# Optimization experiments

Measured on AMD Instinct MI355X. Metric: run time of the kernel, lower is better.

The kernel has to match this reference:

```python
import math
import jax, jax.numpy as jnp
import numpy as np

B, A, M, NC = 32, 8400, 32, 80
TOP_K, ALPHA, BETA, EPS = 13, 1.0, 6.0, 1e-9
IMG = 640.0


def _ciou(b1, b2, eps=1e-7):
    # b1, b2 broadcastable [..., 4]; CIoU as in compute_iou (box1=gt, box2=pred)
    b1x1, b1y1, b1x2, b1y2 = b1[..., 0], b1[..., 1], b1[..., 2], b1[..., 3]
    b2x1, b2y1, b2x2, b2y2 = b2[..., 0], b2[..., 1], b2[..., 2], b2[..., 3]
    w1, h1 = b1x2 - b1x1, b1y2 - b1y1 + eps
    w2, h2 = b2x2 - b2x1, b2y2 - b2y1 + eps
    inter = (jnp.minimum(b1x2, b2x2) - jnp.maximum(b1x1, b2x1)).clip(0) * \
            (jnp.minimum(b1y2, b2y2) - jnp.maximum(b1y1, b2y1)).clip(0)
    union = w1 * h1 + w2 * h2 - inter + eps
    iou = inter / union
    cw = jnp.maximum(b1x2, b2x2) - jnp.minimum(b1x1, b2x1)
    ch = jnp.maximum(b1y2, b2y2) - jnp.minimum(b1y1, b2y1)
    c2 = cw ** 2 + ch ** 2 + eps
    rho2 = ((b2x1 + b2x2 - b1x1 - b1x2) ** 2 + (b2y1 + b2y2 - b1y1 - b1y2) ** 2) / 4.0
    v = (4.0 / math.pi ** 2) * (jnp.arctan(w2 / h2) - jnp.arctan(w1 / h1)) ** 2
    alpha = jax.lax.stop_gradient(v / (v - iou + (1.0 + eps)))
    return iou - (rho2 / c2 + v * alpha)


def setup_inputs() -> dict:
    key = jax.random.key(0)
    ks = jax.random.split(key, 8)
    pd_scores = jax.random.uniform(ks[0], (B, A, NC), jnp.float32)
    anc_points = jax.random.uniform(ks[1], (A, 2), jnp.float32) * IMG
    # predicted boxes around anchor points (valid x1<x2, y1<y2)
    off = jax.random.uniform(ks[2], (B, A, 4), jnp.float32) * 80.0 + 2.0
    pd_bboxes = jnp.concatenate([anc_points[None] - off[..., :2],
                                 anc_points[None] + off[..., 2:]], -1)
    # GT boxes: random centers and sizes, clipped to image
    c = jax.random.uniform(ks[3], (B, M, 2), jnp.float32) * IMG
    wh = jax.random.uniform(ks[4], (B, M, 2), jnp.float32) * 180.0 + 20.0
    gt_bboxes = jnp.concatenate([(c - wh / 2).clip(0, IMG), (c + wh / 2).clip(0, IMG)], -1)
    gt_labels = jax.random.randint(ks[5], (B, M, 1), 0, NC, jnp.int64)
    n_valid = jax.random.randint(ks[6], (B,), 1, M + 1)
    mask_gt = (jnp.arange(M)[None, :] < n_valid[:, None]).astype(jnp.float32)[..., None]
    return {"pd_scores": pd_scores, "pd_bboxes": pd_bboxes, "anc_points": anc_points,
            "gt_labels": gt_labels, "gt_bboxes": gt_bboxes, "mask_gt": mask_gt}


def reference(pd_scores, pd_bboxes, anc_points, gt_labels, gt_bboxes, mask_gt):
    b, a, nc = pd_scores.shape
    m = gt_bboxes.shape[1]
    dtype = pd_scores.dtype

    # anchors-inside-GT mask: [B,M,A]
    lt = gt_bboxes[:, :, None, :2]          # [B,M,1,2]
    rb = gt_bboxes[:, :, None, 2:]
    deltas = jnp.concatenate([anc_points[None, None] - lt,
                              rb - anc_points[None, None]], -1)  # [B,M,A,4]
    mask_in_gts = deltas.min(-1) > EPS
    mg = mask_gt[..., 0] > 0                 # [B,M] bool
    gt_mask = mask_in_gts & mg[:, :, None]

    # per-GT class score gather: pd_scores[b, :, gt_labels[b,m]] -> [B,M,A]
    labels = gt_labels[..., 0]               # [B,M]
    idx = jnp.broadcast_to(labels[:, :, None, None], (b, m, a, 1))
    gathered = jnp.take_along_axis(jnp.broadcast_to(pd_scores[:, None], (b, m, a, nc)), idx, axis=3)[..., 0]
    bbox_scores = jnp.where(gt_mask, gathered, 0.0)

    # CIoU overlaps (dense, masked) [B,M,A]
    iou = _ciou(gt_bboxes[:, :, None, :], pd_bboxes[:, None, :, :])
    overlaps = jnp.where(gt_mask, jnp.maximum(iou, 0.0), 0.0)

    align_metric = bbox_scores ** ALPHA * overlaps ** BETA

    # top-k selection with duplicate suppression (faithful to scatter_add loop)
    _, tk_idx = jax.lax.top_k(align_metric, TOP_K)      # [B,M,K]
    tk_mask = jnp.broadcast_to(mg[:, :, None], tk_idx.shape)
    tk_idx = jnp.where(tk_mask, tk_idx, 0)
    bi = jnp.arange(b)[:, None, None]
    mi = jnp.arange(m)[None, :, None]
    counts = jnp.zeros((b, m, a), jnp.int32).at[bi, mi, tk_idx].add(1)
    mask_top_k = jnp.where(counts > 1, 0, counts).astype(dtype)

    mask_pos = mask_top_k * mask_in_gts.astype(dtype) * mg[:, :, None].astype(dtype)
    fg_mask = mask_pos.sum(1)                            # [B,A]

    # resolve anchors assigned to multiple GTs (no-op when none; matches torch branch)
    mask_multi = fg_mask[:, None, :] > 1                 # [B,M,A] (broadcast)
    max_idx = overlaps.argmax(1)                         # [B,A]
    is_max = (jnp.arange(m)[None, :, None] == max_idx[:, None, :]).astype(dtype)
    mask_pos = jnp.where(mask_multi, is_max, mask_pos)
    fg_mask = mask_pos.sum(1)

    target_gt_idx = mask_pos.argmax(1)                   # [B,A]
    target_labels = jnp.maximum(jnp.take_along_axis(labels, target_gt_idx, axis=1), 0)
    target_bboxes = jnp.take_along_axis(
        gt_bboxes, jnp.broadcast_to(target_gt_idx[..., None], (b, a, 4)), axis=1)

    target_scores = jax.nn.one_hot(target_labels, NC, dtype=dtype)
    target_scores = jnp.where((fg_mask > 0)[..., None], target_scores, 0.0)

    am = align_metric * mask_pos
    pos_am = am.max(-1, keepdims=True)                   # [B,M,1]
    pos_ov = (overlaps * mask_pos).max(-1, keepdims=True)
    norm = (am * pos_ov / (pos_am + EPS)).max(1)[..., None]  # [B,A,1]
    target_scores = target_scores * norm

    return target_bboxes, target_scores, fg_mask > 0
```

## Files before the change

### kernel.cpp

```cpp
#include <hip/hip_runtime.h>
#include <math.h>

#define BB 32
#define AA 8400
#define MM 32
#define NCC 80
#define TOPK 13
#define CAP 1024
#define NW (AA / 32 + 1)
#define K12T 512

typedef float nfloat4 __attribute__((ext_vector_type(4)));

__device__ __forceinline__ void wave_argmax(float& v, int& i) {
    #pragma unroll
    for (int off = 32; off > 0; off >>= 1) {
        float ov = __shfl_xor(v, off, 64);
        int oi = __shfl_xor(i, off, 64);
        if (ov > v || (ov == v && oi < i)) { v = ov; i = oi; }
    }
}

__global__ __launch_bounds__(256) void k0_zero(unsigned int* __restrict__ selmask) {
    int g = blockIdx.x * 256 + threadIdx.x;
    if (g < BB * AA / 4) reinterpret_cast<uint4*>(selmask)[g] = uint4{0u, 0u, 0u, 0u};
}

__global__ __launch_bounds__(K12T) void k12_topk(
        const float* __restrict__ pd_scores, const float* __restrict__ pd_bboxes,
        const float* __restrict__ anc, const int* __restrict__ gt_labels,
        const float* __restrict__ gt_bboxes, const float* __restrict__ mask_gt,
        unsigned int* __restrict__ selmask, float* __restrict__ pos_am, float* __restrict__ pos_ov) {
    __shared__ float lval[CAP];
    __shared__ int   lidx[CAP];
    __shared__ unsigned int bmask[NW];
    __shared__ float wv[8];
    __shared__ int   wi[8];
    __shared__ int   wsum[8];
    __shared__ int   s_p;
    const float eps = 1e-7f;
    int ib = blockIdx.x;
    int b = (ib & 7) + ((ib >> 8) << 3);
    int m = (ib >> 3) & 31;
    int bm = b * MM + m;
    unsigned int mbit = 1u << m;
    int tid = threadIdx.x;
    int lane = tid & 63;
    int wid = tid >> 6;
    if (tid == 0) pos_am[bm] = 0.f;
    if (tid == 1) pos_ov[bm] = 0.f;
    if (tid == 2) s_p = 0;
    if (!(mask_gt[bm] > 0.f)) return;

    for (int i = tid; i < NW; i += K12T) bmask[i] = 0u;
    float4 g = reinterpret_cast<const float4*>(gt_bboxes)[bm];

    const float4* anc4 = reinterpret_cast<const float4*>(anc);
    float4 av[9];
    #pragma unroll
    for (int j = 0; j < 9; j++) {
        int e = tid + (j << 9);
        av[j] = anc4[e > 4199 ? 4199 : e];
    }
    unsigned int bits = 0u;
    int c_t = 0;
    #pragma unroll
    for (int j = 0; j < 9; j++) {
        int e = tid + (j << 9);
        bool valid = e < 4200;
        float d0 = fminf(fminf(av[j].x - g.x, av[j].y - g.y), fminf(g.z - av[j].x, g.w - av[j].y));
        float d1 = fminf(fminf(av[j].z - g.x, av[j].w - g.y), fminf(g.z - av[j].z, g.w - av[j].w));
        if (valid && d0 > 1e-9f) { bits |= 1u << (2 * j);     c_t++; }
        if (valid && d1 > 1e-9f) { bits |= 1u << (2 * j + 1); c_t++; }
    }
    int x = c_t;
    #pragma unroll
    for (int off = 1; off < 64; off <<= 1) {
        int y = __shfl_up(x, off, 64);
        if (lane >= off) x += y;
    }
    if (lane == 63) wsum[wid] = x;
    __syncthreads();
    int base = 0, tot = 0;
    #pragma unroll
    for (int w = 0; w < 8; w++) { if (w < wid) base += wsum[w]; tot += wsum[w]; }
    int n_c = min(tot, CAP);
    {
        int o = base + x - c_t;
        unsigned int mm_ = bits;
        while (mm_) {
            int k = __builtin_ctz(mm_);
            mm_ &= mm_ - 1u;
            int i = 2 * tid + ((k >> 1) << 10) + (k & 1);
            if (o < CAP) lidx[o] = i;
            o++;
        }
    }
    for (int s = n_c + tid; s < CAP; s += K12T) { lval[s] = -1.f; lidx[s] = AA; }
    __syncthreads();

    float w1 = g.z - g.x, h1 = g.w - g.y + eps;
    float atg = atanf(w1 / h1);
    float w1h1 = w1 * h1;
    float sgx = g.x + g.z, sgy = g.y + g.w;
    int lab = gt_labels[bm];
    const float4* pbb = reinterpret_cast<const float4*>(pd_bboxes) + (long)b * AA;
    const float* scp = pd_scores + (long)b * AA * NCC + lab;
    int nit = (n_c + K12T - 1) >> 9;
    for (int it = 0; it < nit; it++) {
        int s = (it << 9) + tid;
        bool pos = false;
        if (s < n_c) {
            int i = lidx[s];
            float4 pb = pbb[i];
            float sc = scp[(long)i * NCC];
            float w2 = pb.z - pb.x, h2 = pb.w - pb.y + eps;
            float iw = fmaxf(fminf(g.z, pb.z) - fmaxf(g.x, pb.x), 0.f);
            float ih = fmaxf(fminf(g.w, pb.w) - fmaxf(g.y, pb.y), 0.f);
            float inter = iw * ih;
            float uni = w1h1 + w2 * h2 - inter + eps;
            float iou = inter / uni;
            float cw = fmaxf(g.z, pb.z) - fminf(g.x, pb.x);
            float ch = fmaxf(g.w, pb.w) - fminf(g.y, pb.y);
            float c2 = cw * cw + ch * ch + eps;
            float dx = pb.x + pb.z - sgx, dy = pb.y + pb.w - sgy;
            float rho2 = (dx * dx + dy * dy) * 0.25f;
            float dv = atanf(w2 / h2) - atg;
            float v = 0.4052847345693511f * dv * dv;
            float alpha = v / (v - iou + (1.0f + eps));
            float cv = iou - (rho2 / c2 + v * alpha);
            float ov = fmaxf(cv, 0.f);
            float o2 = ov * ov;
            float val = sc * o2 * o2 * o2;
            pos = val > 0.f;
            lval[s] = pos ? val : -1.f;
            if (pos) atomicOr(&bmask[i >> 5], 1u << (i & 31));
        }
        unsigned long long pm = __ballot(pos);
        if (lane == 0) atomicAdd(&s_p, (int)__popcll(pm));
    }
    __syncthreads();
    int p = s_p;

    if (p >= TOPK) {
        float v0 = lval[tid], v1 = lval[tid + 512];
        int   i0 = lidx[tid], i1 = lidx[tid + 512];
        int mysel = -1;
        for (int k = 0; k < TOPK; k++) {
            float bv = v0; int bi = i0;
            if (v1 > bv || (v1 == bv && i1 < bi)) { bv = v1; bi = i1; }
            wave_argmax(bv, bi);
            if (lane == 0) { wv[wid] = bv; wi[wid] = bi; }
            __syncthreads();
            float gv = wv[0]; int gi = wi[0];
            #pragma unroll
            for (int w = 1; w < 8; w++) {
                float ov = wv[w]; int oi = wi[w];
                if (ov > gv || (ov == gv && oi < gi)) { gv = ov; gi = oi; }
            }
            if (tid == k) mysel = gi;
            if (i0 == gi) v0 = -1.f;
            if (i1 == gi) v1 = -1.f;
            __syncthreads();
        }
        if (tid < TOPK) atomicOr(&selmask[b * AA + mysel], mbit);
    } else {
        for (int s = tid; s < n_c; s += K12T)
            if (lval[s] > 0.f) atomicOr(&selmask[b * AA + lidx[s]], mbit);
        if (wid == 0) {
            int need = TOPK - p;
            for (int base_i = 0; need > 0 && base_i < AA; base_i += 64) {
                int i = base_i + lane;
                bool cand = (i < AA) && !((bmask[i >> 5] >> (i & 31)) & 1u);
                unsigned long long wm = __ballot(cand);
                int take = min(need, (int)__popcll(wm));
                if (cand && (int)__popcll(wm & ((1ull << lane) - 1ull)) < take) {
                    float2 an = reinterpret_cast<const float2*>(anc)[i];
                    float dmin = fminf(fminf(an.x - g.x, an.y - g.y), fminf(g.z - an.x, g.w - an.y));
                    if (dmin > 1e-9f) atomicOr(&selmask[b * AA + i], mbit);
                }
                need -= take;
            }
        }
    }
}

__global__ __launch_bounds__(256) void k3_resolve(
        const float* __restrict__ pd_scores, const float* __restrict__ pd_bboxes,
        const float* __restrict__ anc, const int* __restrict__ gt_labels,
        const float* __restrict__ gt_bboxes, const float* __restrict__ mask_gt,
        const unsigned int* __restrict__ selmask,
        float* __restrict__ pos_am, float* __restrict__ pos_ov,
        float* __restrict__ out_bbox, float* __restrict__ out_fg,
        int2* __restrict__ meta) {
    __shared__ float sg[MM][8];
    __shared__ int slab[MM];
    __shared__ int smg[MM];
    const float eps = 1e-7f;
    int b = blockIdx.y;
    int tid = threadIdx.x;
    if (tid < MM) {
        int gm = b * MM + tid;
        float4 g = reinterpret_cast<const float4*>(gt_bboxes)[gm];
        float w1 = g.z - g.x, h1 = g.w - g.y + eps;
        sg[tid][0] = g.x; sg[tid][1] = g.y; sg[tid][2] = g.z; sg[tid][3] = g.w;
        sg[tid][4] = w1 * h1;
        sg[tid][5] = atanf(w1 / h1);
        sg[tid][6] = g.x + g.z;
        sg[tid][7] = g.y + g.w;
        int lb = gt_labels[gm]; if (lb < 0) lb = 0;
        slab[tid] = lb;
        smg[tid] = mask_gt[gm] > 0.f ? 1 : 0;
    }
    __syncthreads();
    int a = blockIdx.x * 256 + tid;
    if (a >= AA) return;
    int g = b * AA + a;
    unsigned int sel = selmask[g];
    int fg = __popc(sel);

    int tg = 0; bool fgo = false; float ovt = 0.f;
    if (fg >= 1) {
        float ax = anc[a * 2], ay = anc[a * 2 + 1];
        float4 pb = reinterpret_cast<const float4*>(pd_bboxes)[g];
        float w2 = pb.z - pb.x, h2 = pb.w - pb.y + eps;
        float atp = atanf(w2 / h2);
        float w2h2 = w2 * h2;
        float spx = pb.x + pb.z, spy = pb.y + pb.w;
        fgo = true;
        if (fg == 1) {
            tg = __ffs(sel) - 1;
            float gx1 = sg[tg][0], gy1 = sg[tg][1], gx2 = sg[tg][2], gy2 = sg[tg][3];
            float iw = fmaxf(fminf(gx2, pb.z) - fmaxf(gx1, pb.x), 0.f);
            float ih = fmaxf(fminf(gy2, pb.w) - fmaxf(gy1, pb.y), 0.f);
            float inter = iw * ih;
            float uni = sg[tg][4] + w2h2 - inter + eps;
            float iou = inter / uni;
            float cw = fmaxf(gx2, pb.z) - fminf(gx1, pb.x);
            float ch = fmaxf(gy2, pb.w) - fminf(gy1, pb.y);
            float c2 = cw * cw + ch * ch + eps;
            float dx = spx - sg[tg][6], dy = spy - sg[tg][7];
            float rho2 = (dx * dx + dy * dy) * 0.25f;
            float dv = atp - sg[tg][5];
            float v = 0.4052847345693511f * dv * dv;
            float alpha = v / (v - iou + (1.0f + eps));
            ovt = fmaxf(iou - (rho2 / c2 + v * alpha), 0.f);
        } else {
            float bestov = -1.f; int bestm = 0;
            for (int mm = 0; mm < MM; mm++) {
                float gx1 = sg[mm][0], gy1 = sg[mm][1], gx2 = sg[mm][2], gy2 = sg[mm][3];
                float dmin = fminf(fminf(ax - gx1, ay - gy1), fminf(gx2 - ax, gy2 - ay));
                float ov = 0.f;
                if ((dmin > 1e-9f) && smg[mm]) {
                    float iw = fmaxf(fminf(gx2, pb.z) - fmaxf(gx1, pb.x), 0.f);
                    float ih = fmaxf(fminf(gy2, pb.w) - fmaxf(gy1, pb.y), 0.f);
                    float inter = iw * ih;
                    float uni = sg[mm][4] + w2h2 - inter + eps;
                    float iou = inter / uni;
                    float cw = fmaxf(gx2, pb.z) - fminf(gx1, pb.x);
                    float ch = fmaxf(gy2, pb.w) - fminf(gy1, pb.y);
                    float c2 = cw * cw + ch * ch + eps;
                    float dx = spx - sg[mm][6], dy = spy - sg[mm][7];
                    float rho2 = (dx * dx + dy * dy) * 0.25f;
                    float dv = atp - sg[mm][5];
                    float v = 0.4052847345693511f * dv * dv;
                    float alpha = v / (v - iou + (1.0f + eps));
                    ov = fmaxf(iou - (rho2 / c2 + v * alpha), 0.f);
                }
                if (ov > bestov) { bestov = ov; bestm = mm; }
            }
            tg = bestm; ovt = bestov;
        }
    }

    nfloat4 gb = {sg[tg][0], sg[tg][1], sg[tg][2], sg[tg][3]};
    __builtin_nontemporal_store(gb, reinterpret_cast<nfloat4*>(out_bbox) + g);
    out_fg[g] = fgo ? 1.f : 0.f;
    float amv = 0.f;
    if (fgo) {
        float sc = pd_scores[(long)g * NCC + slab[tg]];
        float o2 = ovt * ovt;
        amv = sc * o2 * o2 * o2;
        atomicMax((int*)&pos_am[b * MM + tg], __float_as_int(amv));
        atomicMax((int*)&pos_ov[b * MM + tg], __float_as_int(ovt));
    }
    meta[g] = make_int2(__float_as_int(amv), tg | (slab[tg] << 8) | ((fgo ? 1 : 0) << 16));
}

__global__ __launch_bounds__(256) void k4_scores(
        const int2* __restrict__ meta,
        const float* __restrict__ pos_am, const float* __restrict__ pos_ov,
        float* __restrict__ out_scores) {
    int g = blockIdx.x * 256 + threadIdx.x;
    const int NQ = NCC / 4;
    if (g >= BB * AA * NQ) return;
    int ba = g / NQ;
    int c0 = (g % NQ) * 4;
    nfloat4 o = {0.f, 0.f, 0.f, 0.f};
    int2 mt = meta[ba];
    int p = mt.y;
    if (p & (1 << 16)) {
        int tg = p & 31, lab = (p >> 8) & 127;
        int b = ba / AA;
        int bm = b * MM + tg;
        float nv = (__int_as_float(mt.x) * pos_ov[bm]) / (pos_am[bm] + 1e-9f);
        int d = lab - c0;
        if (d == 0) o.x = nv; else if (d == 1) o.y = nv;
        else if (d == 2) o.z = nv; else if (d == 3) o.w = nv;
    }
    __builtin_nontemporal_store(o, reinterpret_cast<nfloat4*>(out_scores) + g);
}

extern "C" void kernel_launch(void* const* d_in, const int* in_sizes, int n_in,
                              void* d_out, int out_size, void* d_ws, size_t ws_size,
                              hipStream_t stream) {
    const float* pd_scores = (const float*)d_in[0];
    const float* pd_bboxes = (const float*)d_in[1];
    const float* anc       = (const float*)d_in[2];
    const int*   gt_labels = (const int*)d_in[3];
    const float* gt_bboxes = (const float*)d_in[4];
    const float* mask_gt   = (const float*)d_in[5];

    const long nBA = (long)BB * AA;

    char* ws = (char*)d_ws;
    unsigned int* selmask = (unsigned int*)ws;  ws += nBA * 4;
    float* pos_am = (float*)ws;                 ws += BB * MM * 4;
    float* pos_ov = (float*)ws;                 ws += BB * MM * 4;
    int2*  meta   = (int2*)ws;                  ws += nBA * 8;

    float* out_bbox   = (float*)d_out;
    float* out_scores = out_bbox + nBA * 4;
    float* out_fg     = out_scores + nBA * NCC;

    k0_zero<<<(int)((nBA / 4 + 255) / 256), 256, 0, stream>>>(selmask);
    k12_topk<<<BB * MM, K12T, 0, stream>>>(pd_scores, pd_bboxes, anc, gt_labels,
                                           gt_bboxes, mask_gt, selmask, pos_am, pos_ov);
    dim3 g3((AA + 255) / 256, BB);
    k3_resolve<<<g3, 256, 0, stream>>>(pd_scores, pd_bboxes, anc, gt_labels,
                                       gt_bboxes, mask_gt, selmask, pos_am, pos_ov,
                                       out_bbox, out_fg, meta);
    long nS4 = nBA * (NCC / 4);
    k4_scores<<<(int)((nS4 + 255) / 256), 256, 0, stream>>>(meta, pos_am, pos_ov, out_scores);
}
```

Before: 195.0 us.

## Process two GTs per block and do wave-local top-k selection

The top-k kernel now handles two ground-truth boxes per block. It scans every anchor once, sharing the anchor and predicted-box loads and the predicted-box arctangent between both GTs. The prefix-sum compaction is replaced by shared-memory atomic slot allocation. Top-k selection now runs inside one wave per GT, with 16 values per lane and no block-wide barriers. The cost is that every block loads all predicted boxes rather than only those for candidate anchors, plus contention on the shared-memory atomics.

```diff
diff --git a/kernel.cpp b/kernel.cpp
--- a/kernel.cpp
+++ b/kernel.cpp
@@ -7,8 +7,7 @@
 #define NCC 80
 #define TOPK 13
 #define CAP 1024
-#define NW (AA / 32 + 1)
-#define K12T 512
+#define NW2 ((AA + 31) / 32)
 
 typedef float nfloat4 __attribute__((ext_vector_type(4)));
 
@@ -26,160 +25,141 @@
     if (g < BB * AA / 4) reinterpret_cast<uint4*>(selmask)[g] = uint4{0u, 0u, 0u, 0u};
 }
 
-__global__ __launch_bounds__(K12T) void k12_topk(
+__global__ __launch_bounds__(512) void k12_topk(
         const float* __restrict__ pd_scores, const float* __restrict__ pd_bboxes,
         const float* __restrict__ anc, const int* __restrict__ gt_labels,
         const float* __restrict__ gt_bboxes, const float* __restrict__ mask_gt,
         unsigned int* __restrict__ selmask, float* __restrict__ pos_am, float* __restrict__ pos_ov) {
-    __shared__ float lval[CAP];
-    __shared__ int   lidx[CAP];
-    __shared__ unsigned int bmask[NW];
-    __shared__ float wv[8];
-    __shared__ int   wi[8];
-    __shared__ int   wsum[8];
-    __shared__ int   s_p;
+    __shared__ float lv[2][CAP];
+    __shared__ int   li[2][CAP];
+    __shared__ unsigned int bmask[2][NW2];
+    __shared__ float sg[2][8];
+    __shared__ int   smg[2], slab[2];
+    __shared__ int   cnt[2], pcnt[2];
     const float eps = 1e-7f;
-    int ib = blockIdx.x;
-    int b = (ib & 7) + ((ib >> 8) << 3);
-    int m = (ib >> 3) & 31;
-    int bm = b * MM + m;
-    unsigned int mbit = 1u << m;
+    int blk = blockIdx.x;
+    int b  = blk >> 4;
+    int m0 = (blk & 15) << 1;
     int tid = threadIdx.x;
     int lane = tid & 63;
     int wid = tid >> 6;
-    if (tid == 0) pos_am[bm] = 0.f;
-    if (tid == 1) pos_ov[bm] = 0.f;
-    if (tid == 2) s_p = 0;
-    if (!(mask_gt[bm] > 0.f)) return;
-
-    for (int i = tid; i < NW; i += K12T) bmask[i] = 0u;
-    float4 g = reinterpret_cast<const float4*>(gt_bboxes)[bm];
-
-    const float4* anc4 = reinterpret_cast<const float4*>(anc);
-    float4 av[9];
-    #pragma unroll
-    for (int j = 0; j < 9; j++) {
-        int e = tid + (j << 9);
-        av[j] = anc4[e > 4199 ? 4199 : e];
-    }
-    unsigned int bits = 0u;
-    int c_t = 0;
-    #pragma unroll
-    for (int j = 0; j < 9; j++) {
-        int e = tid + (j << 9);
-        bool valid = e < 4200;
-        float d0 = fminf(fminf(av[j].x - g.x, av[j].y - g.y), fminf(g.z - av[j].x, g.w - av[j].y));
-        float d1 = fminf(fminf(av[j].z - g.x, av[j].w - g.y), fminf(g.z - av[j].z, g.w - av[j].w));
-        if (valid && d0 > 1e-9f) { bits |= 1u << (2 * j);     c_t++; }
-        if (valid && d1 > 1e-9f) { bits |= 1u << (2 * j + 1); c_t++; }
-    }
-    int x = c_t;
-    #pragma unroll
-    for (int off = 1; off < 64; off <<= 1) {
-        int y = __shfl_up(x, off, 64);
-        if (lane >= off) x += y;
-    }
-    if (lane == 63) wsum[wid] = x;
+
+    if (tid < 2) {
+        int bm = b * MM + m0 + tid;
+        pos_am[bm] = 0.f;
+        pos_ov[bm] = 0.f;
+        cnt[tid] = 0; pcnt[tid] = 0;
+        int mgv = mask_gt[bm] > 0.f ? 1 : 0;
+        smg[tid] = mgv;
+        float4 g = reinterpret_cast<const float4*>(gt_bboxes)[bm];
+        float w1 = g.z - g.x, h1 = g.w - g.y + eps;
+        sg[tid][0] = g.x; sg[tid][1] = g.y; sg[tid][2] = g.z; sg[tid][3] = g.w;
+        sg[tid][4] = w1 * h1;
+        sg[tid][5] = atanf(w1 / h1);
+        sg[tid][6] = g.x + g.z;
+        sg[tid][7] = g.y + g.w;
+        slab[tid] = gt_labels[bm];
+    }
+    for (int i = tid; i < 2 * NW2; i += 512) bmask[i >> 8 >> 1][i % NW2] = 0u;
     __syncthreads();
-    int base = 0, tot = 0;
-    #pragma unroll
-    for (int w = 0; w < 8; w++) { if (w < wid) base += wsum[w]; tot += wsum[w]; }
-    int n_c = min(tot, CAP);
-    {
-        int o = base + x - c_t;
-        unsigned int mm_ = bits;
-        while (mm_) {
-            int k = __builtin_ctz(mm_);
-            mm_ &= mm_ - 1u;
-            int i = 2 * tid + ((k >> 1) << 10) + (k & 1);
-            if (o < CAP) lidx[o] = i;
-            o++;
+    for (int i = tid; i < NW2; i += 512) { bmask[0][i] = 0u; bmask[1][i] = 0u; }
+    int mg0 = smg[0], mg1 = smg[1];
+    __syncthreads();
+    if (!mg0 && !mg1) return;
+
+    const float2* anc2 = reinterpret_cast<const float2*>(anc);
+    const float4* pbb = reinterpret_cast<const float4*>(pd_bboxes) + (long)b * AA;
+    const float* scb = pd_scores + (long)b * AA * NCC;
+    #pragma unroll 1
+    for (int j = 0; j < 17; j++) {
+        int i = tid + (j << 9);
+        if (i >= AA) break;
+        float2 an = anc2[i];
+        float4 pb = pbb[i];
+        float w2 = pb.z - pb.x, h2 = pb.w - pb.y + eps;
+        float w2h2 = w2 * h2;
+        float spx = pb.x + pb.z, spy = pb.y + pb.w;
+        float atp = 0.f; bool atp_done = false;
+        #pragma unroll
+        for (int mm = 0; mm < 2; mm++) {
+            if (!(mm ? mg1 : mg0)) continue;
+            float gx1 = sg[mm][0], gy1 = sg[mm][1], gx2 = sg[mm][2], gy2 = sg[mm][3];
+            float dmin = fminf(fminf(an.x - gx1, an.y - gy1), fminf(gx2 - an.x, gy2 - an.y));
+            if (dmin > 1e-9f) {
+                if (!atp_done) { atp = atanf(w2 / h2); atp_done = true; }
+                float iw = fmaxf(fminf(gx2, pb.z) - fmaxf(gx1, pb.x), 0.f);
+                float ih = fmaxf(fminf(gy2, pb.w) - fmaxf(gy1, pb.y), 0.f);
+                float inter = iw * ih;
+                float uni = sg[mm][4] + w2h2 - inter + eps;
+                float iou = inter / uni;
+                float cw = fmaxf(gx2, pb.z) - fminf(gx1, pb.x);
+                float ch = fmaxf(gy2, pb.w) - fminf(gy1, pb.y);
+                float c2 = cw * cw + ch * ch + eps;
+                float dx = spx - sg[mm][6], dy = spy - sg[mm][7];
+                float rho2 = (dx * dx + dy * dy) * 0.25f;
+                float dv = atp - sg[mm][5];
+                float v = 0.4052847345693511f * dv * dv;
+                float alpha = v / (v - iou + (1.0f + eps));
+                float cv = iou - (rho2 / c2 + v * alpha);
+                float ov = fmaxf(cv, 0.f);
+                float sc = scb[(long)i * NCC + slab[mm]];
+                float o2 = ov * ov;
+                float val = sc * o2 * o2 * o2;
+                int slot = atomicAdd(&cnt[mm], 1);
+                bool pos = val > 0.f;
+                if (slot < CAP) { lv[mm][slot] = pos ? val : -1.f; li[mm][slot] = i; }
+                if (pos) {
+                    atomicOr(&bmask[mm][i >> 5], 1u << (i & 31));
+                    atomicAdd(&pcnt[mm], 1);
+                }
+            }
         }
     }
-    for (int s = n_c + tid; s < CAP; s += K12T) { lval[s] = -1.f; lidx[s] = AA; }
     __syncthreads();
 
-    float w1 = g.z - g.x, h1 = g.w - g.y + eps;
-    float atg = atanf(w1 / h1);
-    float w1h1 = w1 * h1;
-    float sgx = g.x + g.z, sgy = g.y + g.w;
-    int lab = gt_labels[bm];
-    const float4* pbb = reinterpret_cast<const float4*>(pd_bboxes) + (long)b * AA;
-    const float* scp = pd_scores + (long)b * AA * NCC + lab;
-    int nit = (n_c + K12T - 1) >> 9;
-    for (int it = 0; it < nit; it++) {
-        int s = (it << 9) + tid;
-        bool pos = false;
-        if (s < n_c) {
-            int i = lidx[s];
-            float4 pb = pbb[i];
-            float sc = scp[(long)i * NCC];
-            float w2 = pb.z - pb.x, h2 = pb.w - pb.y + eps;
-            float iw = fmaxf(fminf(g.z, pb.z) - fmaxf(g.x, pb.x), 0.f);
-            float ih = fmaxf(fminf(g.w, pb.w) - fmaxf(g.y, pb.y), 0.f);
-            float inter = iw * ih;
-            float uni = w1h1 + w2 * h2 - inter + eps;
-            float iou = inter / uni;
-            float cw = fmaxf(g.z, pb.z) - fminf(g.x, pb.x);
-            float ch = fmaxf(g.w, pb.w) - fminf(g.y, pb.y);
-            float c2 = cw * cw + ch * ch + eps;
-            float dx = pb.x + pb.z - sgx, dy = pb.y + pb.w - sgy;
-            float rho2 = (dx * dx + dy * dy) * 0.25f;
-            float dv = atanf(w2 / h2) - atg;
-            float v = 0.4052847345693511f * dv * dv;
-            float alpha = v / (v - iou + (1.0f + eps));
-            float cv = iou - (rho2 / c2 + v * alpha);
-            float ov = fmaxf(cv, 0.f);
-            float o2 = ov * ov;
-            float val = sc * o2 * o2 * o2;
-            pos = val > 0.f;
-            lval[s] = pos ? val : -1.f;
-            if (pos) atomicOr(&bmask[i >> 5], 1u << (i & 31));
-        }
-        unsigned long long pm = __ballot(pos);
-        if (lane == 0) atomicAdd(&s_p, (int)__popcll(pm));
-    }
-    __syncthreads();
-    int p = s_p;
-
-    if (p >= TOPK) {
-        float v0 = lval[tid], v1 = lval[tid + 512];
-        int   i0 = lidx[tid], i1 = lidx[tid + 512];
-        int mysel = -1;
-        for (int k = 0; k < TOPK; k++) {
-            float bv = v0; int bi = i0;
-            if (v1 > bv || (v1 == bv && i1 < bi)) { bv = v1; bi = i1; }
-            wave_argmax(bv, bi);
-            if (lane == 0) { wv[wid] = bv; wi[wid] = bi; }
-            __syncthreads();
-            float gv = wv[0]; int gi = wi[0];
-            #pragma unroll
-            for (int w = 1; w < 8; w++) {
-                float ov = wv[w]; int oi = wi[w];
-                if (ov > gv || (ov == gv && oi < gi)) { gv = ov; gi = oi; }
-            }
-            if (tid == k) mysel = gi;
-            if (i0 == gi) v0 = -1.f;
-            if (i1 == gi) v1 = -1.f;
-            __syncthreads();
-        }
-        if (tid < TOPK) atomicOr(&selmask[b * AA + mysel], mbit);
-    } else {
-        for (int s = tid; s < n_c; s += K12T)
-            if (lval[s] > 0.f) atomicOr(&selmask[b * AA + lidx[s]], mbit);
-        if (wid == 0) {
-            int need = TOPK - p;
-            for (int base_i = 0; need > 0 && base_i < AA; base_i += 64) {
-                int i = base_i + lane;
-                bool cand = (i < AA) && !((bmask[i >> 5] >> (i & 31)) & 1u);
-                unsigned long long wm = __ballot(cand);
-                int take = min(need, (int)__popcll(wm));
-                if (cand && (int)__popcll(wm & ((1ull << lane) - 1ull)) < take) {
-                    float2 an = reinterpret_cast<const float2*>(anc)[i];
-                    float dmin = fminf(fminf(an.x - g.x, an.y - g.y), fminf(g.z - an.x, g.w - an.y));
-                    if (dmin > 1e-9f) atomicOr(&selmask[b * AA + i], mbit);
-                }
-                need -= take;
+    if (wid < 2) {
+        int mm = wid;
+        if (mm ? mg1 : mg0) {
+            unsigned int mbit = 1u << (m0 + mm);
+            int nc = min(cnt[mm], CAP);
+            int p = pcnt[mm];
+            if (p >= TOPK) {
+                float v[16]; int id[16];
+                #pragma unroll
+                for (int j = 0; j < 16; j++) {
+                    int s = lane + (j << 6);
+                    v[j]  = (s < nc) ? lv[mm][s] : -1.f;
+                    id[j] = (s < nc) ? li[mm][s] : AA;
+                }
+                int win = AA;
+                for (int k = 0; k < TOPK; k++) {
+                    float bv = v[0]; int bi = id[0];
+                    #pragma unroll
+                    for (int j = 1; j < 16; j++)
+                        if (v[j] > bv || (v[j] == bv && id[j] < bi)) { bv = v[j]; bi = id[j]; }
+                    wave_argmax(bv, bi);
+                    if (lane == k) win = bi;
+                    #pragma unroll
+                    for (int j = 0; j < 16; j++) if (id[j] == bi) v[j] = -1.f;
+                }
+                if (lane < TOPK) atomicOr(&selmask[b * AA + win], mbit);
+            } else {
+                for (int s = lane; s < nc; s += 64)
+                    if (lv[mm][s] > 0.f) atomicOr(&selmask[b * AA + li[mm][s]], mbit);
+                int need = TOPK - p;
+                float gx1 = sg[mm][0], gy1 = sg[mm][1], gx2 = sg[mm][2], gy2 = sg[mm][3];
+                for (int base_i = 0; need > 0 && base_i < AA; base_i += 64) {
+                    int i = base_i + lane;
+                    bool cand = (i < AA) && !((bmask[mm][i >> 5] >> (i & 31)) & 1u);
+                    unsigned long long wm = __ballot(cand);
+                    int take = min(need, (int)__popcll(wm));
+                    if (cand && (int)__popcll(wm & ((1ull << lane) - 1ull)) < take) {
+                        float2 an = anc2[i];
+                        float dmin = fminf(fminf(an.x - gx1, an.y - gy1), fminf(gx2 - an.x, gy2 - an.y));
+                        if (dmin > 1e-9f) atomicOr(&selmask[b * AA + i], mbit);
+                    }
+                    need -= take;
+                }
             }
         }
     }
@@ -334,8 +314,8 @@
     float* out_fg     = out_scores + nBA * NCC;
 
     k0_zero<<<(int)((nBA / 4 + 255) / 256), 256, 0, stream>>>(selmask);
-    k12_topk<<<BB * MM, K12T, 0, stream>>>(pd_scores, pd_bboxes, anc, gt_labels,
-                                           gt_bboxes, mask_gt, selmask, pos_am, pos_ov);
+    k12_topk<<<BB * 16, 512, 0, stream>>>(pd_scores, pd_bboxes, anc, gt_labels,
+                                          gt_bboxes, mask_gt, selmask, pos_am, pos_ov);
     dim3 g3((AA + 255) / 256, BB);
     k3_resolve<<<g3, 256, 0, stream>>>(pd_scores, pd_bboxes, anc, gt_labels,
                                        gt_bboxes, mask_gt, selmask, pos_am, pos_ov,
```

Result: slower. 208.7 us (+7.0%).
